# Performance work log

Measured on AMD Instinct MI355X. Metric: run time of the kernel, lower is better.

Reference implementation:

```python
import jax, jax.numpy as jnp
import numpy as np

EPS = 1e-7  # keras K.epsilon()


def setup_inputs() -> dict:
    key = jax.random.key(0)
    k1, k2, k3, k4 = jax.random.split(key, 4)
    B, T, D, E = 32, 4096, 512, 512
    x = jax.random.normal(k1, (B, T, D), dtype=jnp.float32)
    y = jax.random.normal(k2, (B, E), dtype=jnp.float32)
    W = jax.random.normal(k3, (D, E), dtype=jnp.float32) * (1.0 / np.sqrt(E))
    b = jnp.zeros((1,), dtype=jnp.float32)
    mask = jax.random.randint(k4, (B, T), 0, 2).astype(bool)
    return {"x": x, "y": y, "W": W, "b": b, "mask": mask}


def reference(x, y, W, b, mask):
    # y' = (W @ y^T)^T = y @ W^T  -> [B, D]
    yp = jnp.matmul(y, W.T)
    # broadcast dot-product score over steps: [B, T]
    eij = jnp.einsum('btd,bd->bt', x, yp) + b  # b is (1,), broadcast over T
    a = jnp.exp(jnp.tanh(eij)) * mask.astype(x.dtype)
    a = a / (jnp.sum(a, axis=1, keepdims=True) + EPS)
    return a
```

## Files before the change

kernel.cpp:

```cpp
#include <hip/hip_runtime.h>

#define B_DIM 32
#define T_DIM 4096
#define D_DIM 512
#define E_DIM 512
#define EPS_K 1e-7f

__global__ __launch_bounds__(256) void yp_kernel(const float* __restrict__ y,
                                                 const float* __restrict__ W,
                                                 float* __restrict__ yp) {
    const int b    = blockIdx.y;
    const int wave = threadIdx.x >> 6;
    const int lane = threadIdx.x & 63;
    const int d    = blockIdx.x * 4 + wave;

    const float4* Wv = (const float4*)(W + (size_t)d * E_DIM);
    const float4* yv = (const float4*)(y + (size_t)b * E_DIM);
    const float4 w0 = Wv[lane];
    const float4 w1 = Wv[lane + 64];
    const float4 y0 = yv[lane];
    const float4 y1 = yv[lane + 64];

    float p = w0.x * y0.x + w0.y * y0.y + w0.z * y0.z + w0.w * y0.w
            + w1.x * y1.x + w1.y * y1.y + w1.z * y1.z + w1.w * y1.w;
#pragma unroll
    for (int off = 32; off > 0; off >>= 1) p += __shfl_xor(p, off);

    if (lane == 0) yp[(size_t)b * D_DIM + d] = p;
}

__global__ __launch_bounds__(256) void score_kernel(const float* __restrict__ x,
                                                    const float* __restrict__ yp,
                                                    const float* __restrict__ bias,
                                                    const int* __restrict__ mask,
                                                    float* __restrict__ a_raw) {
    const int b    = blockIdx.y;
    const int wave = threadIdx.x >> 6;
    const int lane = threadIdx.x & 63;
    const int t0   = blockIdx.x * 32 + wave * 8;

    const float4* ypv = (const float4*)(yp + (size_t)b * D_DIM);
    const float4 w0 = ypv[lane];
    const float4 w1 = ypv[lane + 64];

    const float4* xv = (const float4*)(x + ((size_t)b * T_DIM + (size_t)t0) * D_DIM);

    float4 xa[8], xb[8];
#pragma unroll
    for (int i = 0; i < 8; ++i) {
        xa[i] = xv[i * (D_DIM / 4) + lane];
        xb[i] = xv[i * (D_DIM / 4) + lane + 64];
    }

    float p[8];
#pragma unroll
    for (int i = 0; i < 8; ++i) {
        p[i] = xa[i].x * w0.x + xa[i].y * w0.y + xa[i].z * w0.z + xa[i].w * w0.w
             + xb[i].x * w1.x + xb[i].y * w1.y + xb[i].z * w1.z + xb[i].w * w1.w;
    }

#pragma unroll
    for (int off = 32; off > 0; off >>= 1) {
#pragma unroll
        for (int i = 0; i < 8; ++i) p[i] += __shfl_xor(p[i], off);
    }

    if (lane < 8) {
        float s = (lane == 0) ? p[0] : (lane == 1) ? p[1] : (lane == 2) ? p[2]
                : (lane == 3) ? p[3] : (lane == 4) ? p[4] : (lane == 5) ? p[5]
                : (lane == 6) ? p[6] : p[7];
        const int t = t0 + lane;
        const float e = expf(tanhf(s + bias[0]));
        const float a = mask[(size_t)b * T_DIM + t] ? e : 0.f;
        a_raw[(size_t)b * T_DIM + t] = a;
    }
}

__global__ __launch_bounds__(1024) void norm_kernel(const float* __restrict__ a_raw,
                                                    float* __restrict__ out) {
    const int b   = blockIdx.x;
    const int tid = threadIdx.x;
    const float4 v = ((const float4*)(a_raw + (size_t)b * T_DIM))[tid];
    float s = v.x + v.y + v.z + v.w;
#pragma unroll
    for (int off = 32; off > 0; off >>= 1) s += __shfl_xor(s, off);

    __shared__ float wsum[16];
    __shared__ float inv_s;
    const int wave = tid >> 6;
    const int lane = tid & 63;
    if (lane == 0) wsum[wave] = s;
    __syncthreads();
    if (tid == 0) {
        float tot = 0.f;
        for (int i = 0; i < 16; ++i) tot += wsum[i];
        inv_s = 1.0f / (tot + EPS_K);
    }
    __syncthreads();
    const float inv = inv_s;
    const float4 o = make_float4(v.x * inv, v.y * inv, v.z * inv, v.w * inv);
    ((float4*)(out + (size_t)b * T_DIM))[tid] = o;
}

extern "C" void kernel_launch(void* const* d_in, const int* in_sizes, int n_in,
                              void* d_out, int out_size, void* d_ws, size_t ws_size,
                              hipStream_t stream) {
    const float* x    = (const float*)d_in[0];
    const float* y    = (const float*)d_in[1];
    const float* W    = (const float*)d_in[2];
    const float* bias = (const float*)d_in[3];
    const int*   mask = (const int*)d_in[4];
    float* out = (float*)d_out;

    float* yp    = (float*)d_ws;
    float* a_raw = yp + B_DIM * D_DIM;

    yp_kernel<<<dim3(D_DIM / 4, B_DIM), 256, 0, stream>>>(y, W, yp);
    score_kernel<<<dim3(T_DIM / 32, B_DIM), 256, 0, stream>>>(x, yp, bias, mask, a_raw);
    norm_kernel<<<B_DIM, 1024, 0, stream>>>(a_raw, out);
}
```

Before: 50.81 us.

## Fuse projection, scoring and normalization into one cooperative persistent kernel

Replaces the three-kernel pipeline with a single cooperative kernel that computes yp, the masked scores with per-block partial sums, and the final normalization, separated by grid-wide syncs. This removes two launch boundaries and the full re-reduction of a_raw in the norm step by summing partials during scoring. The cost is grid.sync overhead and a persistent loop that may keep fewer x loads in flight than the original oversubscribed grid. It falls back to the old kernels if the cooperative launch fails.

```diff
diff --git a/kernel.cpp b/kernel.cpp
--- a/kernel.cpp
+++ b/kernel.cpp
@@ -1,10 +1,125 @@
 #include <hip/hip_runtime.h>
+#include <hip/hip_cooperative_groups.h>
+
+namespace cg = cooperative_groups;
 
 #define B_DIM 32
 #define T_DIM 4096
 #define D_DIM 512
 #define E_DIM 512
 #define EPS_K 1e-7f
+
+__global__ __launch_bounds__(256, 4) void fused_kernel(
+    const float* __restrict__ x, const float* __restrict__ y,
+    const float* __restrict__ W, const float* __restrict__ bias,
+    const int* __restrict__ mask, float* __restrict__ out,
+    float* __restrict__ yp, float* __restrict__ a_raw,
+    float* __restrict__ partials) {
+
+    const int wave = threadIdx.x >> 6;
+    const int lane = threadIdx.x & 63;
+    const int nblk = gridDim.x;
+    __shared__ float ls[4];
+    __shared__ float inv_s;
+    cg::grid_group grid = cg::this_grid();
+
+    for (int gw = blockIdx.x * 4 + wave; gw < 4096; gw += nblk * 4) {
+        const int idx0 = gw * 4;
+        const int b0   = idx0 >> 9;
+        const int d0   = idx0 & 511;
+        const float4* yv = (const float4*)(y + (size_t)b0 * E_DIM);
+        const float4 y0 = yv[lane];
+        const float4 y1 = yv[lane + 64];
+        float acc[4];
+#pragma unroll
+        for (int k = 0; k < 4; ++k) {
+            const float4* Wv = (const float4*)(W + (size_t)(d0 + k) * E_DIM);
+            const float4 w0 = Wv[lane];
+            const float4 w1 = Wv[lane + 64];
+            acc[k] = w0.x*y0.x + w0.y*y0.y + w0.z*y0.z + w0.w*y0.w
+                   + w1.x*y1.x + w1.y*y1.y + w1.z*y1.z + w1.w*y1.w;
+        }
+#pragma unroll
+        for (int off = 32; off > 0; off >>= 1) {
+#pragma unroll
+            for (int k = 0; k < 4; ++k) acc[k] += __shfl_xor(acc[k], off);
+        }
+        if (lane == 0)
+            *(float4*)(yp + idx0) = make_float4(acc[0], acc[1], acc[2], acc[3]);
+    }
+
+    grid.sync();
+
+    for (int task = blockIdx.x; task < 1024; task += nblk) {
+        const int b     = task >> 5;
+        const int tbase = (task & 31) * 128;
+        const float4* ypv = (const float4*)(yp + (size_t)b * D_DIM);
+        const float4 w0 = ypv[lane];
+        const float4 w1 = ypv[lane + 64];
+        const float bv = bias[0];
+        float bsum = 0.f;
+
+#pragma unroll
+        for (int i = 0; i < 4; ++i) {
+            const int t0 = tbase + wave * 32 + i * 8;
+            const float4* xv = (const float4*)(x + ((size_t)b * T_DIM + t0) * D_DIM);
+            float4 xa[8], xb[8];
+#pragma unroll
+            for (int j = 0; j < 8; ++j) {
+                xa[j] = xv[j * (D_DIM / 4) + lane];
+                xb[j] = xv[j * (D_DIM / 4) + lane + 64];
+            }
+            float p[8];
+#pragma unroll
+            for (int j = 0; j < 8; ++j) {
+                p[j] = xa[j].x*w0.x + xa[j].y*w0.y + xa[j].z*w0.z + xa[j].w*w0.w
+                     + xb[j].x*w1.x + xb[j].y*w1.y + xb[j].z*w1.z + xb[j].w*w1.w;
+            }
+#pragma unroll
+            for (int off = 32; off > 0; off >>= 1) {
+#pragma unroll
+                for (int j = 0; j < 8; ++j) p[j] += __shfl_xor(p[j], off);
+            }
+            float a = 0.f;
+            if (lane < 8) {
+                float s = (lane==0)?p[0]:(lane==1)?p[1]:(lane==2)?p[2]:(lane==3)?p[3]
+                        :(lane==4)?p[4]:(lane==5)?p[5]:(lane==6)?p[6]:p[7];
+                const int t = t0 + lane;
+                const float e = expf(tanhf(s + bv));
+                a = mask[(size_t)b * T_DIM + t] ? e : 0.f;
+                a_raw[(size_t)b * T_DIM + t] = a;
+            }
+            bsum += a;
+        }
+
+#pragma unroll
+        for (int off = 32; off > 0; off >>= 1) bsum += __shfl_xor(bsum, off);
+        if (lane == 0) ls[wave] = bsum;
+        __syncthreads();
+        if (threadIdx.x == 0)
+            partials[task] = (ls[0] + ls[1]) + (ls[2] + ls[3]);
+        __syncthreads();
+    }
+
+    grid.sync();
+
+    for (int task = blockIdx.x; task < 128; task += nblk) {
+        const int b = task >> 2;
+        if (threadIdx.x < 32) {
+            float s = partials[b * 32 + threadIdx.x];
+#pragma unroll
+            for (int off = 16; off > 0; off >>= 1) s += __shfl_xor(s, off);
+            if (threadIdx.x == 0) inv_s = 1.0f / (s + EPS_K);
+        }
+        __syncthreads();
+        const float inv = inv_s;
+        const int idx = (task & 3) * 256 + threadIdx.x;
+        const float4 v = ((const float4*)(a_raw + (size_t)b * T_DIM))[idx];
+        ((float4*)(out + (size_t)b * T_DIM))[idx] =
+            make_float4(v.x * inv, v.y * inv, v.z * inv, v.w * inv);
+        __syncthreads();
+    }
+}
 
 __global__ __launch_bounds__(256) void yp_kernel(const float* __restrict__ y,
                                                  const float* __restrict__ W,
@@ -13,19 +128,16 @@
     const int wave = threadIdx.x >> 6;
     const int lane = threadIdx.x & 63;
     const int d    = blockIdx.x * 4 + wave;
-
     const float4* Wv = (const float4*)(W + (size_t)d * E_DIM);
     const float4* yv = (const float4*)(y + (size_t)b * E_DIM);
     const float4 w0 = Wv[lane];
     const float4 w1 = Wv[lane + 64];
     const float4 y0 = yv[lane];
     const float4 y1 = yv[lane + 64];
-
-    float p = w0.x * y0.x + w0.y * y0.y + w0.z * y0.z + w0.w * y0.w
-            + w1.x * y1.x + w1.y * y1.y + w1.z * y1.z + w1.w * y1.w;
+    float p = w0.x*y0.x + w0.y*y0.y + w0.z*y0.z + w0.w*y0.w
+            + w1.x*y1.x + w1.y*y1.y + w1.z*y1.z + w1.w*y1.w;
 #pragma unroll
     for (int off = 32; off > 0; off >>= 1) p += __shfl_xor(p, off);
-
     if (lane == 0) yp[(size_t)b * D_DIM + d] = p;
 }
 
@@ -38,41 +150,33 @@
     const int wave = threadIdx.x >> 6;
     const int lane = threadIdx.x & 63;
     const int t0   = blockIdx.x * 32 + wave * 8;
-
     const float4* ypv = (const float4*)(yp + (size_t)b * D_DIM);
     const float4 w0 = ypv[lane];
     const float4 w1 = ypv[lane + 64];
-
     const float4* xv = (const float4*)(x + ((size_t)b * T_DIM + (size_t)t0) * D_DIM);
-
     float4 xa[8], xb[8];
 #pragma unroll
     for (int i = 0; i < 8; ++i) {
         xa[i] = xv[i * (D_DIM / 4) + lane];
         xb[i] = xv[i * (D_DIM / 4) + lane + 64];
     }
-
     float p[8];
 #pragma unroll
     for (int i = 0; i < 8; ++i) {
-        p[i] = xa[i].x * w0.x + xa[i].y * w0.y + xa[i].z * w0.z + xa[i].w * w0.w
-             + xb[i].x * w1.x + xb[i].y * w1.y + xb[i].z * w1.z + xb[i].w * w1.w;
-    }
-
+        p[i] = xa[i].x*w0.x + xa[i].y*w0.y + xa[i].z*w0.z + xa[i].w*w0.w
+             + xb[i].x*w1.x + xb[i].y*w1.y + xb[i].z*w1.z + xb[i].w*w1.w;
+    }
 #pragma unroll
     for (int off = 32; off > 0; off >>= 1) {
 #pragma unroll
         for (int i = 0; i < 8; ++i) p[i] += __shfl_xor(p[i], off);
     }
-
     if (lane < 8) {
-        float s = (lane == 0) ? p[0] : (lane == 1) ? p[1] : (lane == 2) ? p[2]
-                : (lane == 3) ? p[3] : (lane == 4) ? p[4] : (lane == 5) ? p[5]
-                : (lane == 6) ? p[6] : p[7];
+        float s = (lane==0)?p[0]:(lane==1)?p[1]:(lane==2)?p[2]:(lane==3)?p[3]
+                :(lane==4)?p[4]:(lane==5)?p[5]:(lane==6)?p[6]:p[7];
         const int t = t0 + lane;
         const float e = expf(tanhf(s + bias[0]));
-        const float a = mask[(size_t)b * T_DIM + t] ? e : 0.f;
-        a_raw[(size_t)b * T_DIM + t] = a;
+        a_raw[(size_t)b * T_DIM + t] = mask[(size_t)b * T_DIM + t] ? e : 0.f;
     }
 }
 
@@ -84,12 +188,9 @@
     float s = v.x + v.y + v.z + v.w;
 #pragma unroll
     for (int off = 32; off > 0; off >>= 1) s += __shfl_xor(s, off);
-
     __shared__ float wsum[16];
     __shared__ float inv_s;
-    const int wave = tid >> 6;
-    const int lane = tid & 63;
-    if (lane == 0) wsum[wave] = s;
+    if ((tid & 63) == 0) wsum[tid >> 6] = s;
     __syncthreads();
     if (tid == 0) {
         float tot = 0.f;
@@ -98,8 +199,8 @@
     }
     __syncthreads();
     const float inv = inv_s;
-    const float4 o = make_float4(v.x * inv, v.y * inv, v.z * inv, v.w * inv);
-    ((float4*)(out + (size_t)b * T_DIM))[tid] = o;
+    ((float4*)(out + (size_t)b * T_DIM))[tid] =
+        make_float4(v.x * inv, v.y * inv, v.z * inv, v.w * inv);
 }
 
 extern "C" void kernel_launch(void* const* d_in, const int* in_sizes, int n_in,
@@ -112,8 +213,22 @@
     const int*   mask = (const int*)d_in[4];
     float* out = (float*)d_out;
 
-    float* yp    = (float*)d_ws;
-    float* a_raw = yp + B_DIM * D_DIM;
+    float* yp       = (float*)d_ws;
+    float* a_raw    = yp + B_DIM * D_DIM;
+    float* partials = a_raw + B_DIM * T_DIM;
+
+    int occ = 0;
+    hipError_t oe = hipOccupancyMaxActiveBlocksPerMultiprocessor(&occ, fused_kernel, 256, 0);
+    if (oe == hipSuccess && occ >= 1) {
+        int nblk = occ * 256;
+        if (nblk > 1024) nblk = 1024;
+        void* args[] = {(void*)&x, (void*)&y, (void*)&W, (void*)&bias,
+                        (void*)&mask, (void*)&out, (void*)&yp, (void*)&a_raw,
+                        (void*)&partials};
+        hipError_t le = hipLaunchCooperativeKernel(fused_kernel, dim3(nblk),
+                                                   dim3(256), args, 0u, stream);
+        if (le == hipSuccess) return;
+    }
 
     yp_kernel<<<dim3(D_DIM / 4, B_DIM), 256, 0, stream>>>(y, W, yp);
     score_kernel<<<dim3(T_DIM / 32, B_DIM), 256, 0, stream>>>(x, yp, bias, mask, a_raw);
```

Result: slower. 147.8 us (+191.0%).
